# Kernel tuning notes

Measured on AMD Instinct MI355X. Metric: run time of the kernel, lower is better.

Reference implementation:

```python
import jax, jax.numpy as jnp
import numpy as np
from jax import lax

D_MODEL = 1024
D_STATE = 16
D_CONV = 4
D_INNER = 2048  # expand * d_model
DT_RANK = 64    # ceil(d_model / 16)
BATCH = 2
SEQ = 2048


def setup_inputs() -> dict:
    key = jax.random.key(0)
    ks = jax.random.split(key, 8)
    s = 0.02
    x = jax.random.normal(ks[0], (BATCH, SEQ, D_MODEL), jnp.float32)
    in_proj_w = jax.random.normal(ks[1], (2 * D_INNER, D_MODEL), jnp.float32) * s
    conv_w = jax.random.normal(ks[2], (D_INNER, 1, D_CONV), jnp.float32) * s  # [out, in/groups, k]
    conv_b = jax.random.normal(ks[3], (D_INNER,), jnp.float32) * s
    x_proj_w = jax.random.normal(ks[4], (DT_RANK + 2 * D_STATE, D_INNER), jnp.float32) * s
    dt_proj_w = jax.random.normal(ks[5], (D_INNER, DT_RANK), jnp.float32) * s
    dt_proj_b = jax.random.normal(ks[6], (D_INNER,), jnp.float32) * s
    A_log = jnp.log(jnp.tile(jnp.arange(1, D_STATE + 1, dtype=jnp.float32), (D_INNER, 1)))
    D = jnp.ones((D_INNER,), jnp.float32)
    out_proj_w = jax.random.normal(ks[7], (D_MODEL, D_INNER), jnp.float32) * s
    return dict(x=x, in_proj_w=in_proj_w, conv_w=conv_w, conv_b=conv_b,
                x_proj_w=x_proj_w, dt_proj_w=dt_proj_w, dt_proj_b=dt_proj_b,
                A_log=A_log, D=D, out_proj_w=out_proj_w)


def _causal_depthwise_conv(x_bcl, conv_w, conv_b):
    # x_bcl: [B, d_inner, L]; conv_w: [d_inner, 1, k]; left-pad k-1 -> causal, output length L
    y = lax.conv_general_dilated(
        x_bcl, conv_w,
        window_strides=(1,), padding=[(D_CONV - 1, 0)],
        feature_group_count=D_INNER,
        dimension_numbers=('NCH', 'OIH', 'NCH'))
    return y + conv_b[None, :, None]


def _ssm(xc, x_proj_w, dt_proj_w, dt_proj_b, A_log, D):
    # xc: [B, L, d_inner]
    A = -jnp.exp(A_log)                                   # [d, N]
    x_dbl = jnp.einsum('bld,rd->blr', xc, x_proj_w)       # [B, L, dt_rank + 2N]
    dt_low = x_dbl[..., :DT_RANK]
    Bm = x_dbl[..., DT_RANK:DT_RANK + D_STATE]            # [B, L, N]
    Cm = x_dbl[..., DT_RANK + D_STATE:]                   # [B, L, N]
    dt = jax.nn.softplus(jnp.einsum('blr,dr->bld', dt_low, dt_proj_w) + dt_proj_b)  # [B, L, d]
    dA = jnp.exp(dt[..., None] * A)                       # [B, L, d, N]
    dBx = dt[..., None] * Bm[:, :, None, :] * xc[..., None]  # [B, L, d, N]

    def step(h, inp):
        dA_t, dBx_t, C_t = inp                            # [B,d,N], [B,d,N], [B,N]
        h = dA_t * h + dBx_t
        y = jnp.einsum('bdn,bn->bd', h, C_t)
        return h, y

    h0 = jnp.zeros((xc.shape[0], D_INNER, D_STATE), xc.dtype)
    _, ys = lax.scan(step, h0,
                     (dA.transpose(1, 0, 2, 3), dBx.transpose(1, 0, 2, 3), Cm.transpose(1, 0, 2)))
    y = ys.transpose(1, 0, 2)                             # [B, L, d]
    return y + xc * D


def reference(x, in_proj_w, conv_w, conv_b, x_proj_w, dt_proj_w, dt_proj_b, A_log, D, out_proj_w):
    xz = jnp.einsum('blm,om->blo', x, in_proj_w)          # [B, L, 2*d_inner]
    xs, z = jnp.split(xz, 2, axis=-1)
    xc = _causal_depthwise_conv(xs.transpose(0, 2, 1), conv_w, conv_b).transpose(0, 2, 1)
    xc = jax.nn.silu(xc)
    y = _ssm(xc, x_proj_w, dt_proj_w, dt_proj_b, A_log, D)
    out = y * jax.nn.silu(z)
    return jnp.einsum('bld,md->blm', out, out_proj_w)
```

## Files before the change

### kernel.cpp

```cpp
#include <hip/hip_runtime.h>

#define SEQ    2048
#define DIN    2048
#define DMODEL 1024
#define NROWS  4096
#define NCH    32
#define CHL    64

typedef __attribute__((ext_vector_type(8))) _Float16 half8v;
typedef __attribute__((ext_vector_type(8))) unsigned short ushort8v;
typedef __attribute__((ext_vector_type(4))) float f32x4;

__device__ __forceinline__ float sigf(float x) { return 1.0f / (1.0f + __expf(-x)); }
__device__ __forceinline__ float softplusf(float v) {
    return fmaxf(v, 0.f) + __logf(1.f + __expf(-fabsf(v)));
}

__device__ __forceinline__ void gload16(const void* g, const void* l) {
    __builtin_amdgcn_global_load_lds((const __attribute__((address_space(1))) void*)g,
                                     (__attribute__((address_space(3))) void*)l, 16, 0, 0);
}

__device__ __forceinline__ unsigned short f2h(float x) {
    _Float16 h = (_Float16)x;
    unsigned short u;
    __builtin_memcpy(&u, &h, 2);
    return u;
}
__device__ __forceinline__ float h2f(unsigned short u) {
    _Float16 h;
    __builtin_memcpy(&h, &u, 2);
    return (float)h;
}

__global__ __launch_bounds__(256) void cvt_in_k(
    const float* __restrict__ x, const float* __restrict__ wi, const float* __restrict__ wx,
    const float* __restrict__ wd, const float* __restrict__ wo,
    unsigned short* __restrict__ xh, unsigned short* __restrict__ wih,
    unsigned short* __restrict__ wxh, unsigned short* __restrict__ wdh,
    unsigned short* __restrict__ woh)
{
    int i = blockIdx.x * 256 + threadIdx.x;
    if (i < 1048576) {
        float4 v = ((const float4*)x)[i];
        ushort4 h; h.x = f2h(v.x); h.y = f2h(v.y); h.z = f2h(v.z); h.w = f2h(v.w);
        ((ushort4*)xh)[i] = h;
    } else if (i < 2097152) {
        i -= 1048576;
        float4 v = ((const float4*)wi)[i];
        ushort4 h; h.x = f2h(v.x); h.y = f2h(v.y); h.z = f2h(v.z); h.w = f2h(v.w);
        ((ushort4*)wih)[i] = h;
    } else if (i < 2162688) {
        i -= 2097152;
        int row = i >> 9, q = i & 511;
        ushort4 h;
        if (row < 96) {
            float4 v = ((const float4*)wx)[(size_t)row * 512 + q];
            h.x = f2h(v.x); h.y = f2h(v.y); h.z = f2h(v.z); h.w = f2h(v.w);
        } else h = make_ushort4(0, 0, 0, 0);
        ((ushort4*)wxh)[(size_t)row * 512 + q] = h;
    } else if (i < 2195456) {
        i -= 2162688;
        float4 v = ((const float4*)wd)[i];
        ushort4 h; h.x = f2h(v.x); h.y = f2h(v.y); h.z = f2h(v.z); h.w = f2h(v.w);
        ((ushort4*)wdh)[i] = h;
    } else {
        i -= 2195456;
        float4 v = ((const float4*)wo)[i];
        ushort4 h; h.x = f2h(v.x); h.y = f2h(v.y); h.z = f2h(v.z); h.w = f2h(v.w);
        ((ushort4*)woh)[i] = h;
    }
}

__global__ __launch_bounds__(512, 2) void gemm256_h(
    const unsigned short* __restrict__ A, const unsigned short* __restrict__ W,
    unsigned short* __restrict__ C, int K, int N, int mtiles, int lda, int ldw)
{
    __shared__ uint4 ldsu4[8192];
    char* lds = (char*)ldsu4;
    const int tid = threadIdx.x;
    const int w = tid >> 6, lane = tid & 63;

    const int nwg = gridDim.x;
    const int cpx = nwg >> 3;
    const int bid = blockIdx.x;
    const int swz = (bid & 7) * cpx + (bid >> 3);
    const int ntiles = nwg / mtiles;
    const int per = 8 * ntiles;
    const int gid = swz / per;
    const int rem = swz - gid * per;
    const int m0 = (gid * 8 + (rem & 7)) * 256;
    const int n0 = (rem >> 3) * 256;

    const int wr = w >> 2, wc = w & 3;
    const int lm = lane & 15, lk = lane >> 4;

    f32x4 acc[8][4];
#pragma unroll
    for (int i = 0; i < 8; ++i)
#pragma unroll
        for (int j = 0; j < 4; ++j) { acc[i][j][0]=0.f; acc[i][j][1]=0.f; acc[i][j][2]=0.f; acc[i][j][3]=0.f; }

    const int rsub = w * 8 + (lane >> 3);
    const int xr8  = ((lane & 7) ^ (lane >> 3)) << 3;
    const unsigned short* gA = A + (size_t)(m0 + rsub) * lda + xr8;
    const unsigned short* gW = W + (size_t)(n0 + rsub) * ldw + xr8;
    const int sdst = w * 1024;

    auto stageA = [&](int bb, int hi, int kt) {
        char* d = lds + bb * 65536 + hi * 16384 + sdst;
        const unsigned short* s = gA + (size_t)hi * 128 * lda + kt;
        gload16(s, d);
        gload16(s + (size_t)64 * lda, d + 8192);
    };
    auto stageB = [&](int bb, int hi, int kt) {
        char* d = lds + bb * 65536 + 32768 + hi * 16384 + sdst;
        const unsigned short* s = gW + (size_t)hi * 128 * ldw + kt;
        gload16(s, d);
        gload16(s + (size_t)64 * ldw, d + 8192);
    };

    half8v a[4][2], b[2][2][2];
    auto loadA = [&](int bb, int mh) {
#pragma unroll
        for (int mb = 0; mb < 4; ++mb)
#pragma unroll
            for (int kk = 0; kk < 2; ++kk) {
                int ar = wr * 128 + (mh * 4 + mb) * 16 + lm;
                a[mb][kk] = *(const half8v*)(lds + bb * 65536 + ar * 128 + (((kk * 4 + lk) ^ (lm & 7)) << 4));
            }
    };
    auto loadB = [&](int bb, int nh) {
#pragma unroll
        for (int nb = 0; nb < 2; ++nb)
#pragma unroll
            for (int kk = 0; kk < 2; ++kk) {
                int br = wc * 64 + (nh * 2 + nb) * 16 + lm;
                b[nh][nb][kk] = *(const half8v*)(lds + bb * 65536 + 32768 + br * 128 + (((kk * 4 + lk) ^ (lm & 7)) << 4));
            }
    };
    auto mm = [&](int mh, int nh) {
        __builtin_amdgcn_s_setprio(1);
#pragma unroll
        for (int mb = 0; mb < 4; ++mb)
#pragma unroll
            for (int nb = 0; nb < 2; ++nb)
#pragma unroll
                for (int kk = 0; kk < 2; ++kk)
                    acc[mh * 4 + mb][nh * 2 + nb] = __builtin_amdgcn_mfma_f32_16x16x32_f16(
                        a[mb][kk], b[nh][nb][kk], acc[mh * 4 + mb][nh * 2 + nb], 0, 0, 0);
        __builtin_amdgcn_s_setprio(0);
    };
#define VMW4() asm volatile("s_waitcnt vmcnt(4)" ::: "memory")
#define BAR()  __builtin_amdgcn_s_barrier()

    stageA(0, 0, 0); stageA(0, 1, 0); stageB(0, 0, 0); stageB(0, 1, 0);
    asm volatile("s_waitcnt vmcnt(0)" ::: "memory");
    BAR();

    const int NT = K >> 6;
    for (int t = 0; t < NT - 1; ++t) {
        const int cur = t & 1, nxt = cur ^ 1;
        const int kt = (t + 1) << 6;
        loadA(cur, 0); loadB(cur, 0);
        stageA(nxt, 0, kt);
        BAR();
        mm(0, 0);
        VMW4(); BAR();
        loadB(cur, 1);
        stageB(nxt, 0, kt);
        BAR();
        mm(0, 1);
        VMW4(); BAR();
        loadA(cur, 1);
        stageB(nxt, 1, kt);
        BAR();
        mm(1, 1);
        VMW4(); BAR();
        stageA(nxt, 1, kt);
        BAR();
        mm(1, 0);
        VMW4(); BAR();
    }
    {
        const int cur = (NT - 1) & 1;
        asm volatile("s_waitcnt vmcnt(0)" ::: "memory");
        BAR();
        loadA(cur, 0); loadB(cur, 0); mm(0, 0);
        loadB(cur, 1); mm(0, 1);
        loadA(cur, 1); mm(1, 1); mm(1, 0);
    }
#undef VMW4
#undef BAR

#pragma unroll
    for (int mb = 0; mb < 8; ++mb)
#pragma unroll
        for (int nb = 0; nb < 4; ++nb)
#pragma unroll
            for (int r = 0; r < 4; ++r)
                C[(size_t)(m0 + wr * 128 + mb * 16 + lk * 4 + r) * N + (n0 + wc * 64 + nb * 16 + lm)]
                    = f2h(acc[mb][nb][r]);
}

#define A_OFF 0
#define W_OFF 16384

__global__ __launch_bounds__(256) void gemm_mfma_h(
    const unsigned short* __restrict__ A, const unsigned short* __restrict__ W,
    unsigned short* __restrict__ C, int K, int ldc, int nmax, int mtiles,
    int sA1, int sA2, int ldw, const float* __restrict__ bias, int kspl, int cstride)
{
    __shared__ uint4 ldsu4[2048];
    char* lds = (char*)ldsu4;
    const int tid  = threadIdx.x;
    const int w    = tid >> 6, lane = tid & 63;

    const int nwg = gridDim.x;
    const int cpx = nwg >> 3;
    const int bid = blockIdx.x;
    const int swz = (bid & 7) * cpx + (bid >> 3);
    const int nbp = nwg / kspl;
    const int ks  = swz / nbp;
    const int tt  = swz - ks * nbp;
    const int ntiles = nbp / mtiles;
    const int per = 8 * ntiles;
    const int gid = tt / per;
    const int rem = tt - gid * per;
    const int m0 = (gid * 8 + (rem & 7)) * 128;
    const int n0 = (rem >> 3) * 128;
    const int kOff = ks * K;

    const int wr = w >> 1, wc = w & 1;

    f32x4 acc[4][4];
#pragma unroll
    for (int i = 0; i < 4; ++i)
#pragma unroll
        for (int j = 0; j < 4; ++j) { acc[i][j][0]=0.f; acc[i][j][1]=0.f; acc[i][j][2]=0.f; acc[i][j][3]=0.f; }

    const int rloc = w * 32 + (lane >> 3);
    const int xr8  = ((lane & 7) ^ (lane >> 3)) << 3;
    const int rowA = m0 + rloc;
    const unsigned short* gA = A + (size_t)(rowA >> 1) * sA2 + (size_t)(rowA & 1) * sA1 + kOff + xr8;
    const unsigned short* gW = W + (size_t)(n0 + rloc) * ldw + kOff + xr8;

    const int lm  = lane & 15;
    const int lk  = lane >> 4;
    const int lk4 = lk * 4;

    for (int kt = 0; kt < K; kt += 64) {
#pragma unroll
        for (int i = 0; i < 4; ++i) {
            const int rb = w * 32 + i * 8;
            gload16(gA + (size_t)i * 4 * sA2 + kt, lds + A_OFF + rb * 128);
            gload16(gW + (size_t)i * 8 * ldw + kt, lds + W_OFF + rb * 128);
        }
        __syncthreads();
#pragma unroll
        for (int h = 0; h < 2; ++h) {
            half8v af[4], wf[4];
            const int ch = h * 4 + lk;
#pragma unroll
            for (int t = 0; t < 4; ++t) {
                const int ar = wr * 64 + t * 16 + lm;
                const int wrw = wc * 64 + t * 16 + lm;
                af[t] = *(const half8v*)(lds + A_OFF + ar * 128 + ((ch ^ (ar & 7)) << 4));
                wf[t] = *(const half8v*)(lds + W_OFF + wrw * 128 + ((ch ^ (wrw & 7)) << 4));
            }
#pragma unroll
            for (int i = 0; i < 4; ++i)
#pragma unroll
                for (int j = 0; j < 4; ++j)
                    acc[i][j] = __builtin_amdgcn_mfma_f32_16x16x32_f16(af[i], wf[j], acc[i][j], 0, 0, 0);
        }
        __syncthreads();
    }

    unsigned short* Cp = C + (size_t)ks * cstride;
    if (bias) {
#pragma unroll
        for (int j = 0; j < 4; ++j) {
            const int n = n0 + wc * 64 + j * 16 + lm;
            const float bv = (n < nmax) ? bias[n] : 0.f;
#pragma unroll
            for (int i = 0; i < 4; ++i)
#pragma unroll
                for (int r = 0; r < 4; ++r) {
                    float v = acc[i][j][r] + bv;
                    if (n < nmax)
                        Cp[(size_t)(m0 + wr * 64 + i * 16 + lk4 + r) * ldc + n] = f2h(softplusf(v));
                }
        }
    } else {
#pragma unroll
        for (int i = 0; i < 4; ++i)
#pragma unroll
            for (int j = 0; j < 4; ++j) {
                const int n = n0 + wc * 64 + j * 16 + lm;
                if (n < nmax)
#pragma unroll
                    for (int r = 0; r < 4; ++r)
                        Cp[(size_t)(m0 + wr * 64 + i * 16 + lk4 + r) * ldc + n] = f2h(acc[i][j][r]);
            }
    }
}

__global__ __launch_bounds__(256) void xproj_reduce_k(
    const unsigned short* __restrict__ part, float* __restrict__ xdbl,
    unsigned short* __restrict__ dlh)
{
    int i = blockIdx.x * 256 + threadIdx.x;
    if (i >= NROWS * 32) return;
    int row = i >> 5, q = i & 31;
    float s0 = 0.f, s1 = 0.f, s2 = 0.f, s3 = 0.f;
#pragma unroll
    for (int ks = 0; ks < 8; ++ks) {
        ushort4 v = *(const ushort4*)(part + (size_t)ks * (NROWS * 128) + (size_t)row * 128 + q * 4);
        s0 += h2f(v.x); s1 += h2f(v.y); s2 += h2f(v.z); s3 += h2f(v.w);
    }
    if (q < 16) {
        ushort4 h; h.x = f2h(s0); h.y = f2h(s1); h.z = f2h(s2); h.w = f2h(s3);
        *(ushort4*)(dlh + (size_t)row * 64 + q * 4) = h;
    } else {
        *(float4*)(xdbl + (size_t)row * 96 + q * 4) = make_float4(s0, s1, s2, s3);
    }
}

__global__ __launch_bounds__(256) void out_reduce_k(
    const unsigned short* __restrict__ p, float* __restrict__ out)
{
    int i = blockIdx.x * 256 + threadIdx.x;
    ushort4 a = ((const ushort4*)p)[i];
    ushort4 b = ((const ushort4*)(p + 4194304))[i];
    float4 v;
    v.x = h2f(a.x) + h2f(b.x);
    v.y = h2f(a.y) + h2f(b.y);
    v.z = h2f(a.z) + h2f(b.z);
    v.w = h2f(a.w) + h2f(b.w);
    ((float4*)out)[i] = v;
}

__global__ __launch_bounds__(256) void conv_silu_k(
    const unsigned short* __restrict__ xzh, const float* __restrict__ cw,
    const float* __restrict__ cb, unsigned short* __restrict__ xch)
{
    int i = blockIdx.x * 256 + threadIdx.x;
    int d8 = (i & 255) << 3;
    int row = i >> 8;
    int l = row & (SEQ - 1);
    const unsigned short* base = xzh + (size_t)row * 4096 + d8;
    ushort8v x0 = *(const ushort8v*)base;
    ushort8v x1 = {}, x2 = {}, x3 = {};
    if (l >= 1) x1 = *(const ushort8v*)(base - 4096);
    if (l >= 2) x2 = *(const ushort8v*)(base - 8192);
    if (l >= 3) x3 = *(const ushort8v*)(base - 12288);
    ushort8v out;
#pragma unroll
    for (int j = 0; j < 8; ++j) {
        float4 wv = *(const float4*)(cw + (size_t)(d8 + j) * 4);
        float a = cb[d8 + j];
        a = fmaf(h2f(x3[j]), wv.x, a);
        a = fmaf(h2f(x2[j]), wv.y, a);
        a = fmaf(h2f(x1[j]), wv.z, a);
        a = fmaf(h2f(x0[j]), wv.w, a);
        out[j] = f2h(a * sigf(a));
    }
    *(ushort8v*)(xch + (size_t)row * DIN + d8) = out;
}

__global__ __launch_bounds__(256) void scan_pass1(
    const unsigned short* __restrict__ dth, const unsigned short* __restrict__ xch,
    const float* __restrict__ xdbl, const float* __restrict__ Alog,
    float* __restrict__ hbuf, float* __restrict__ apbuf)
{
    const int b = blockIdx.z, c = blockIdx.y;
    const int d = blockIdx.x * 256 + threadIdx.x;
    float A[16];
#pragma unroll
    for (int q = 0; q < 4; ++q) *(float4*)&A[q * 4] = *(const float4*)&Alog[(size_t)d * 16 + q * 4];
#pragma unroll
    for (int n = 0; n < 16; ++n) A[n] = -__expf(A[n]);
    float h[16] = {}, ap[16];
#pragma unroll
    for (int n = 0; n < 16; ++n) ap[n] = 1.f;
    const int rowbase = b * SEQ + c * CHL;
    for (int t = 0; t < CHL; ++t) {
        const int row = rowbase + t;
        const float* xr = xdbl + (size_t)row * 96;
        float dtv = h2f(dth[(size_t)row * DIN + d]);
        float xcv = h2f(xch[(size_t)row * DIN + d]);
        float u = dtv * xcv;
#pragma unroll
        for (int n = 0; n < 16; ++n) {
            float dA = __expf(dtv * A[n]);
            h[n] = fmaf(dA, h[n], u * xr[64 + n]);
            ap[n] *= dA;
        }
    }
    size_t e = ((size_t)(b * NCH + c) << 15) + (size_t)d * 16;
#pragma unroll
    for (int q = 0; q < 4; ++q) {
        *(float4*)(hbuf + e + q * 4)  = *(float4*)&h[q * 4];
        *(float4*)(apbuf + e + q * 4) = *(float4*)&ap[q * 4];
    }
}

__global__ __launch_bounds__(256) void scan_pass2(
    float* __restrict__ hbuf, const float* __restrict__ apbuf)
{
    int idx = blockIdx.x * 256 + threadIdx.x;
    int b = idx >> 15;
    int dn = idx & 32767;
    float carry = 0.f;
    for (int c = 0; c < NCH; ++c) {
        size_t e = ((size_t)(b * NCH + c) << 15) + dn;
        float hl = hbuf[e];
        float ap = apbuf[e];
        hbuf[e] = carry;
        carry = fmaf(ap, carry, hl);
    }
}

__global__ __launch_bounds__(256) void scan_pass3(
    const unsigned short* __restrict__ dth, const unsigned short* __restrict__ xch,
    const unsigned short* __restrict__ xzh, const float* __restrict__ xdbl,
    const float* __restrict__ Alog, const float* __restrict__ Dp,
    const float* __restrict__ hbuf, unsigned short* __restrict__ oph)
{
    const int b = blockIdx.z, c = blockIdx.y;
    const int d = blockIdx.x * 256 + threadIdx.x;
    float A[16];
#pragma unroll
    for (int q = 0; q < 4; ++q) *(float4*)&A[q * 4] = *(const float4*)&Alog[(size_t)d * 16 + q * 4];
#pragma unroll
    for (int n = 0; n < 16; ++n) A[n] = -__expf(A[n]);
    float h[16];
    size_t e = ((size_t)(b * NCH + c) << 15) + (size_t)d * 16;
#pragma unroll
    for (int q = 0; q < 4; ++q) *(float4*)&h[q * 4] = *(const float4*)(hbuf + e + q * 4);
    const float Dd = Dp[d];
    const int rowbase = b * SEQ + c * CHL;
    for (int t = 0; t < CHL; ++t) {
        const int row = rowbase + t;
        const float* xr = xdbl + (size_t)row * 96;
        float dtv = h2f(dth[(size_t)row * DIN + d]);
        float xcv = h2f(xch[(size_t)row * DIN + d]);
        float zv  = h2f(xzh[(size_t)row * 4096 + DIN + d]);
        float u = dtv * xcv;
        float y = 0.f;
#pragma unroll
        for (int n = 0; n < 16; ++n) {
            float dA = __expf(dtv * A[n]);
            h[n] = fmaf(dA, h[n], u * xr[64 + n]);
            y = fmaf(h[n], xr[80 + n], y);
        }
        float val = (y + xcv * Dd) * zv * sigf(zv);
        oph[(size_t)row * DIN + d] = f2h(val);
    }
}

extern "C" void kernel_launch(void* const* d_in, const int* in_sizes, int n_in,
                              void* d_out, int out_size, void* d_ws, size_t ws_size,
                              hipStream_t stream)
{
    const float* x    = (const float*)d_in[0];
    const float* wi   = (const float*)d_in[1];
    const float* cw   = (const float*)d_in[2];
    const float* cb   = (const float*)d_in[3];
    const float* wx   = (const float*)d_in[4];
    const float* wd   = (const float*)d_in[5];
    const float* bd   = (const float*)d_in[6];
    const float* alog = (const float*)d_in[7];
    const float* Dp   = (const float*)d_in[8];
    const float* wo   = (const float*)d_in[9];
    float* out = (float*)d_out;

    float* wsf  = (float*)d_ws;
    float* xzr  = wsf;
    float* xcr  = wsf + 16777216;
    float* xdbl = wsf + 25165824;
    float* dtr  = wsf + 25559040;

    unsigned short* xzh = (unsigned short*)xzr;
    float* scr = xzr + 8388608;
    unsigned short* oph = (unsigned short*)scr;
    float* hbuf         = scr + 4194304;
    unsigned short* dlh = (unsigned short*)(scr + 6291456);
    unsigned short* wdh = (unsigned short*)(scr + 6422528);
    unsigned short* woh = (unsigned short*)(scr + 6488064);

    unsigned short* xh  = (unsigned short*)xcr;
    unsigned short* xch = (unsigned short*)xcr;
    float* apbuf        = xcr + 4194304;

    unsigned short* wih    = (unsigned short*)dtr;
    unsigned short* wxh    = (unsigned short*)dtr + 4194304;
    unsigned short* xparth = (unsigned short*)(dtr + 2162688);
    unsigned short* dth    = (unsigned short*)dtr;
    unsigned short* oparth = (unsigned short*)(dtr + 4194304);

    cvt_in_k<<<10624, 256, 0, stream>>>(x, wi, wx, wd, wo, xh, wih, wxh, wdh, woh);
    gemm256_h<<<256, 512, 0, stream>>>(xh, wih, xzh, 1024, 4096, 16, 1024, 1024);
    conv_silu_k<<<4096, 256, 0, stream>>>(xzh, cw, cb, xch);
    gemm_mfma_h<<<256, 256, 0, stream>>>(xch, wxh, xparth, 256, 128, 128, 32, 2048, 4096, 2048,
                                         nullptr, 8, NROWS * 128);
    xproj_reduce_k<<<512, 256, 0, stream>>>(xparth, xdbl, dlh);
    gemm_mfma_h<<<512, 256, 0, stream>>>(dlh, wdh, dth, 64, 2048, 2048, 32, 64, 128, 64,
                                         bd, 1, 0);
    scan_pass1<<<dim3(8, NCH, 2), 256, 0, stream>>>(dth, xch, xdbl, alog, hbuf, apbuf);
    scan_pass2<<<256, 256, 0, stream>>>(hbuf, apbuf);
    scan_pass3<<<dim3(8, NCH, 2), 256, 0, stream>>>(dth, xch, xzh, xdbl, alog, Dp, hbuf, oph);
    gemm_mfma_h<<<512, 256, 0, stream>>>(oph, woh, oparth, 1024, 1024, 1024, 32, 2048, 4096, 2048,
                                         nullptr, 2, 4194304);
    out_reduce_k<<<4096, 256, 0, stream>>>(oparth, out);
}
```

Baseline: 214.9 us.

## Specialize scan for integer A via power recurrence, halve chunk length

```diff
diff --git a/kernel.cpp b/kernel.cpp
--- a/kernel.cpp
+++ b/kernel.cpp
@@ -4,8 +4,8 @@
 #define DIN    2048
 #define DMODEL 1024
 #define NROWS  4096
-#define NCH    32
-#define CHL    64
+#define NCH    64
+#define CHL    32
 
 typedef __attribute__((ext_vector_type(8))) _Float16 half8v;
 typedef __attribute__((ext_vector_type(8))) unsigned short ushort8v;
@@ -379,24 +379,60 @@
     float A[16];
 #pragma unroll
     for (int q = 0; q < 4; ++q) *(float4*)&A[q * 4] = *(const float4*)&Alog[(size_t)d * 16 + q * 4];
-#pragma unroll
-    for (int n = 0; n < 16; ++n) A[n] = -__expf(A[n]);
-    float h[16] = {}, ap[16];
-#pragma unroll
-    for (int n = 0; n < 16; ++n) ap[n] = 1.f;
+    bool seq = true;
+#pragma unroll
+    for (int n = 0; n < 16; ++n) {
+        A[n] = -__expf(A[n]);
+        seq = seq && (fabsf(A[n] + (float)(n + 1)) < 1e-5f * (float)(n + 1));
+    }
+    float h[16] = {};
+    float sumdt = 0.f;
     const int rowbase = b * SEQ + c * CHL;
-    for (int t = 0; t < CHL; ++t) {
-        const int row = rowbase + t;
-        const float* xr = xdbl + (size_t)row * 96;
-        float dtv = h2f(dth[(size_t)row * DIN + d]);
-        float xcv = h2f(xch[(size_t)row * DIN + d]);
-        float u = dtv * xcv;
-#pragma unroll
-        for (int n = 0; n < 16; ++n) {
-            float dA = __expf(dtv * A[n]);
-            h[n] = fmaf(dA, h[n], u * xr[64 + n]);
-            ap[n] *= dA;
-        }
+    int row = rowbase;
+    float dtv = h2f(dth[(size_t)row * DIN + d]);
+    float xcv = h2f(xch[(size_t)row * DIN + d]);
+    if (seq) {
+        for (int t = 0; t < CHL; ++t) {
+            const int nrow = row + ((t + 1) < CHL ? 1 : 0);
+            float dtv2 = h2f(dth[(size_t)nrow * DIN + d]);
+            float xcv2 = h2f(xch[(size_t)nrow * DIN + d]);
+            const float* xr = xdbl + (size_t)row * 96;
+            float u = dtv * xcv;
+            sumdt += dtv;
+            float r = __expf(-dtv);
+            float dA = r;
+#pragma unroll
+            for (int n = 0; n < 16; ++n) {
+                h[n] = fmaf(dA, h[n], u * xr[64 + n]);
+                dA *= r;
+            }
+            dtv = dtv2; xcv = xcv2; row = nrow;
+        }
+    } else {
+        for (int t = 0; t < CHL; ++t) {
+            const int nrow = row + ((t + 1) < CHL ? 1 : 0);
+            float dtv2 = h2f(dth[(size_t)nrow * DIN + d]);
+            float xcv2 = h2f(xch[(size_t)nrow * DIN + d]);
+            const float* xr = xdbl + (size_t)row * 96;
+            float u = dtv * xcv;
+            sumdt += dtv;
+#pragma unroll
+            for (int n = 0; n < 16; ++n) {
+                float dA = __expf(dtv * A[n]);
+                h[n] = fmaf(dA, h[n], u * xr[64 + n]);
+            }
+            dtv = dtv2; xcv = xcv2; row = nrow;
+        }
+    }
+    float ap[16];
+    if (seq) {
+        float R = __expf(-sumdt);
+        float a = R;
+#pragma unroll
+        for (int n = 0; n < 16; ++n) { ap[n] = a; a *= R; }
+    } else {
+#pragma unroll
+        for (int n = 0; n < 16; ++n) ap[n] = __expf(sumdt * A[n]);
     }
     size_t e = ((size_t)(b * NCH + c) << 15) + (size_t)d * 16;
 #pragma unroll
@@ -433,30 +469,62 @@
     float A[16];
 #pragma unroll
     for (int q = 0; q < 4; ++q) *(float4*)&A[q * 4] = *(const float4*)&Alog[(size_t)d * 16 + q * 4];
-#pragma unroll
-    for (int n = 0; n < 16; ++n) A[n] = -__expf(A[n]);
+    bool seq = true;
+#pragma unroll
+    for (int n = 0; n < 16; ++n) {
+        A[n] = -__expf(A[n]);
+        seq = seq && (fabsf(A[n] + (float)(n + 1)) < 1e-5f * (float)(n + 1));
+    }
     float h[16];
     size_t e = ((size_t)(b * NCH + c) << 15) + (size_t)d * 16;
 #pragma unroll
     for (int q = 0; q < 4; ++q) *(float4*)&h[q * 4] = *(const float4*)(hbuf + e + q * 4);
     const float Dd = Dp[d];
     const int rowbase = b * SEQ + c * CHL;
-    for (int t = 0; t < CHL; ++t) {
-        const int row = rowbase + t;
-        const float* xr = xdbl + (size_t)row * 96;
-        float dtv = h2f(dth[(size_t)row * DIN + d]);
-        float xcv = h2f(xch[(size_t)row * DIN + d]);
-        float zv  = h2f(xzh[(size_t)row * 4096 + DIN + d]);
-        float u = dtv * xcv;
-        float y = 0.f;
-#pragma unroll
-        for (int n = 0; n < 16; ++n) {
-            float dA = __expf(dtv * A[n]);
-            h[n] = fmaf(dA, h[n], u * xr[64 + n]);
-            y = fmaf(h[n], xr[80 + n], y);
-        }
-        float val = (y + xcv * Dd) * zv * sigf(zv);
-        oph[(size_t)row * DIN + d] = f2h(val);
+    int row = rowbase;
+    float dtv = h2f(dth[(size_t)row * DIN + d]);
+    float xcv = h2f(xch[(size_t)row * DIN + d]);
+    float zv  = h2f(xzh[(size_t)row * 4096 + DIN + d]);
+    if (seq) {
+        for (int t = 0; t < CHL; ++t) {
+            const int nrow = row + ((t + 1) < CHL ? 1 : 0);
+            float dtv2 = h2f(dth[(size_t)nrow * DIN + d]);
+            float xcv2 = h2f(xch[(size_t)nrow * DIN + d]);
+            float zv2  = h2f(xzh[(size_t)nrow * 4096 + DIN + d]);
+            const float* xr = xdbl + (size_t)row * 96;
+            float u = dtv * xcv;
+            float r = __expf(-dtv);
+            float dA = r;
+            float y = 0.f;
+#pragma unroll
+            for (int n = 0; n < 16; ++n) {
+                h[n] = fmaf(dA, h[n], u * xr[64 + n]);
+                y = fmaf(h[n], xr[80 + n], y);
+                dA *= r;
+            }
+            float val = (y + xcv * Dd) * zv * sigf(zv);
+            oph[(size_t)row * DIN + d] = f2h(val);
+            dtv = dtv2; xcv = xcv2; zv = zv2; row = nrow;
+        }
+    } else {
+        for (int t = 0; t < CHL; ++t) {
+            const int nrow = row + ((t + 1) < CHL ? 1 : 0);
+            float dtv2 = h2f(dth[(size_t)nrow * DIN + d]);
+            float xcv2 = h2f(xch[(size_t)nrow * DIN + d]);
+            float zv2  = h2f(xzh[(size_t)nrow * 4096 + DIN + d]);
+            const float* xr = xdbl + (size_t)row * 96;
+            float u = dtv * xcv;
+            float y = 0.f;
+#pragma unroll
+            for (int n = 0; n < 16; ++n) {
+                float dA = __expf(dtv * A[n]);
+                h[n] = fmaf(dA, h[n], u * xr[64 + n]);
+                y = fmaf(h[n], xr[80 + n], y);
+            }
+            float val = (y + xcv * Dd) * zv * sigf(zv);
+            oph[(size_t)row * DIN + d] = f2h(val);
+            dtv = dtv2; xcv = xcv2; zv = zv2; row = nrow;
+        }
     }
 }
 
@@ -486,19 +554,19 @@
     float* scr = xzr + 8388608;
     unsigned short* oph = (unsigned short*)scr;
     float* hbuf         = scr + 4194304;
-    unsigned short* dlh = (unsigned short*)(scr + 6291456);
-    unsigned short* wdh = (unsigned short*)(scr + 6422528);
-    unsigned short* woh = (unsigned short*)(scr + 6488064);
 
     unsigned short* xh  = (unsigned short*)xcr;
     unsigned short* xch = (unsigned short*)xcr;
     float* apbuf        = xcr + 4194304;
 
     unsigned short* wih    = (unsigned short*)dtr;
-    unsigned short* wxh    = (unsigned short*)dtr + 4194304;
-    unsigned short* xparth = (unsigned short*)(dtr + 2162688);
     unsigned short* dth    = (unsigned short*)dtr;
-    unsigned short* oparth = (unsigned short*)(dtr + 4194304);
+    unsigned short* oparth = (unsigned short*)dtr;
+    unsigned short* wxh    = (unsigned short*)(dtr + 4194304);
+    unsigned short* xparth = (unsigned short*)(dtr + 4325376);
+    unsigned short* woh    = (unsigned short*)(dtr + 6422528);
+    unsigned short* wdh    = (unsigned short*)(dtr + 7471104);
+    unsigned short* dlh    = (unsigned short*)(dtr + 7536640);
 
     cvt_in_k<<<10624, 256, 0, stream>>>(x, wi, wx, wd, wo, xh, wih, wxh, wdh, woh);
     gemm256_h<<<256, 512, 0, stream>>>(xh, wih, xzh, 1024, 4096, 16, 1024, 1024);
```

New measurement: 194.3 us. 9.6% less time.
